# Performance work log

Hardware: AMD Instinct MI355X
Metric: run time of the kernel (lower is better)

Reference implementation:

```python
import jax, jax.numpy as jnp
import numpy as np

N, E, F_IN, F_OUT, PERIODS = 40000, 640000, 64, 128, 12


def setup_inputs() -> dict:
    key = jax.random.key(0)
    ks = jax.random.split(key, 24)
    def w(k, shape):
        return jax.random.normal(k, shape, jnp.float32) * 0.05
    inp = {
        "X": jax.random.normal(ks[0], (N, F_IN, PERIODS), jnp.float32),
        "edge_index": jax.random.randint(ks[1], (2, E), 0, N),
        "edge_weight": jax.random.uniform(ks[2], (E,), jnp.float32),
        "attention": jax.random.uniform(ks[3], (PERIODS,), jnp.float32),
    }
    for idx, g in enumerate(["i", "f", "c", "o"]):
        inp[f"W_x{g}"] = w(ks[4 + 4 * idx], (F_IN, F_OUT))
        inp[f"b_x{g}"] = jnp.zeros((F_OUT,), jnp.float32)
        inp[f"W_h{g}"] = w(ks[5 + 4 * idx], (2 * F_OUT, F_OUT))
        inp[f"b_h{g}"] = jnp.zeros((F_OUT,), jnp.float32)
    return inp


def reference(X, edge_index, edge_weight, attention,
              W_xi, b_xi, W_hi, b_hi,
              W_xf, b_xf, W_hf, b_hf,
              W_xc, b_xc, W_hc, b_hc,
              W_xo, b_xo, W_ho, b_ho):
    n = X.shape[0]
    # GCN normalization with self-loops: D^-1/2 (A + I) D^-1/2
    loops = jnp.arange(n)
    rows = jnp.concatenate([edge_index[0], loops])  # sources
    cols = jnp.concatenate([edge_index[1], loops])  # targets
    wts = jnp.concatenate([edge_weight, jnp.ones((n,), X.dtype)])
    deg = jax.ops.segment_sum(wts, cols, num_segments=n)
    dinv = jnp.where(deg > 0, jax.lax.rsqrt(deg), 0.0)
    norm = dinv[rows] * wts * dinv[cols]  # [E+N]

    def gcn(x, W, b):
        xw = x @ W  # [N, F_OUT]
        agg = jax.ops.segment_sum(norm[:, None] * xw[rows], cols, num_segments=n)
        return agg + b

    probs = jax.nn.softmax(attention)
    H0 = jnp.zeros((n, W_hi.shape[1]), X.dtype)
    C0 = jnp.zeros_like(H0)
    Xp = jnp.moveaxis(X, 2, 0)  # [periods, N, F_IN]

    def step(carry, xs):
        H, C, Hacc = carry
        x_t, p = xs
        def gate(Wx, bx, Wh, bh):
            return jnp.concatenate([gcn(x_t, Wx, bx), H], axis=1) @ Wh + bh
        I = jax.nn.sigmoid(gate(W_xi, b_xi, W_hi, b_hi))
        F = jax.nn.sigmoid(gate(W_xf, b_xf, W_hf, b_hf))
        Ct = jnp.tanh(gate(W_xc, b_xc, W_hc, b_hc))
        O = jax.nn.sigmoid(gate(W_xo, b_xo, W_ho, b_ho))
        C_new = F * C + I * Ct
        H_new = O * jnp.tanh(C_new)
        return (H_new, C_new, Hacc + p * H_new), None

    (H, C, Hacc), _ = jax.lax.scan(step, (H0, C0, H0), (Xp, probs))
    return Hacc
```

## Files before the change

### kernel.cpp

```cpp
#include <hip/hip_runtime.h>

typedef __bf16 bf16_t;
typedef bf16_t bf16x4 __attribute__((ext_vector_type(4)));
typedef bf16_t bf16x8 __attribute__((ext_vector_type(8)));
typedef float floatx4 __attribute__((ext_vector_type(4)));

#define F_INq 64
#define F_OUTq 128
#define PERIODSq 12
#define XROW (F_INq * PERIODSq)

__global__ __launch_bounds__(256) void k_init(float* deg, int* counts, int N) {
  int i = blockIdx.x * 256 + threadIdx.x;
  if (i < N) { deg[i] = 1.0f; counts[i] = 0; }
}

__global__ __launch_bounds__(256) void k_accum(const int* __restrict__ ei, const float* __restrict__ ew,
                                               float* deg, int* counts, int E) {
  int e = blockIdx.x * 256 + threadIdx.x;
  if (e < E) {
    int c = ei[E + e];
    atomicAdd(&deg[c], ew[e]);
    atomicAdd(&counts[c], 1);
  }
}

__global__ __launch_bounds__(256) void k_dinv(float* deg, int N) {
  int i = blockIdx.x * 256 + threadIdx.x;
  if (i < N) { float d = deg[i]; deg[i] = d > 0.0f ? rsqrtf(d) : 0.0f; }
}

__global__ __launch_bounds__(256) void k_scanA(const int* __restrict__ counts, float* __restrict__ deg,
                                               int* __restrict__ bsum, int N) {
  __shared__ int ws[4];
  int b = blockIdx.x, t = threadIdx.x;
  int base = b * 1024 + t * 4;
  int s = 0;
  if (base + 3 < N) {
    int4 c = *(const int4*)(counts + base);
    s = c.x + c.y + c.z + c.w;
  } else {
    for (int k = 0; k < 4; ++k) if (base + k < N) s += counts[base + k];
  }
#pragma unroll
  for (int k = 0; k < 4; ++k) {
    int idx = base + k;
    if (idx < N) { float d = deg[idx]; deg[idx] = d > 0.0f ? rsqrtf(d) : 0.0f; }
  }
  for (int off = 1; off < 64; off <<= 1) s += __shfl_xor(s, off);
  int lane = t & 63, w = t >> 6;
  if (lane == 0) ws[w] = s;
  __syncthreads();
  if (t == 0) bsum[b] = ws[0] + ws[1] + ws[2] + ws[3];
}

__global__ __launch_bounds__(256) void k_scanC(const int* __restrict__ counts, const int* __restrict__ bsum,
                                               int* __restrict__ offs, int* __restrict__ cursor, int N, int nb) {
  __shared__ int ws[4];
  int b = blockIdx.x, t = threadIdx.x;
  int base = b * 1024 + t * 4;
  int c0_ = 0, c1_ = 0, c2_ = 0, c3_ = 0;
  if (base + 3 < N) {
    int4 c = *(const int4*)(counts + base);
    c0_ = c.x; c1_ = c.y; c2_ = c.z; c3_ = c.w;
  } else {
    if (base < N) c0_ = counts[base];
    if (base + 1 < N) c1_ = counts[base + 1];
    if (base + 2 < N) c2_ = counts[base + 2];
    if (base + 3 < N) c3_ = counts[base + 3];
  }
  int tot = c0_ + c1_ + c2_ + c3_;
  int lane = t & 63, w = t >> 6;
  int inc = tot;
  for (int off = 1; off < 64; off <<= 1) {
    int u = __shfl_up(inc, off);
    if (lane >= off) inc += u;
  }
  if (lane == 63) ws[w] = inc;
  __syncthreads();
  int wb = 0;
  for (int i = 0; i < b; ++i) wb += bsum[i];
  for (int i = 0; i < w; ++i) wb += ws[i];
  int e = wb + inc - tot;
  if (base < N)     { offs[base] = e;                 cursor[base] = e; }
  if (base + 1 < N) { int o = e + c0_;                offs[base + 1] = o; cursor[base + 1] = o; }
  if (base + 2 < N) { int o = e + c0_ + c1_;          offs[base + 2] = o; cursor[base + 2] = o; }
  if (base + 3 < N) { int o = e + c0_ + c1_ + c2_;    offs[base + 3] = o; cursor[base + 3] = o; }
  if (b == nb - 1 && t == 0) {
    int tt2 = 0;
    for (int i = 0; i < nb - 1; ++i) tt2 += bsum[i];
    offs[N] = tt2 + ws[0] + ws[1] + ws[2] + ws[3];
  }
}

__global__ __launch_bounds__(1024) void k_scan(const int* __restrict__ counts, int* __restrict__ offs,
                                               int* __restrict__ cursor, int N) {
  __shared__ int sd[1024];
  int t = threadIdx.x;
  int CH = (N + 1023) >> 10;
  int base = t * CH;
  int sum = 0;
  for (int i = 0; i < CH; ++i) { int idx = base + i; if (idx < N) sum += counts[idx]; }
  sd[t] = sum;
  __syncthreads();
  for (int off = 1; off < 1024; off <<= 1) {
    int v = (t >= off) ? sd[t - off] : 0;
    __syncthreads();
    sd[t] += v;
    __syncthreads();
  }
  int run = sd[t] - sum;
  for (int i = 0; i < CH; ++i) {
    int idx = base + i;
    if (idx < N) { offs[idx] = run; cursor[idx] = run; run += counts[idx]; }
  }
  if (t == 1023) offs[N] = sd[1023];
}

__global__ __launch_bounds__(256) void k_scatter(const int* __restrict__ ei, const float* __restrict__ ew,
                                                 const float* __restrict__ dinv, int* cursor,
                                                 int* __restrict__ csr_src, float* __restrict__ csr_nrm, int E) {
  int e = blockIdx.x * 256 + threadIdx.x;
  if (e < E) {
    int r = ei[e], c = ei[E + e];
    int p = atomicAdd(&cursor[c], 1);
    csr_src[p] = r;
    csr_nrm[p] = dinv[r] * ew[e] * dinv[c];
  }
}

__global__ __launch_bounds__(256) void k_prew(
    const float* __restrict__ Wxi, const float* __restrict__ Whi,
    const float* __restrict__ Wxf, const float* __restrict__ Whf,
    const float* __restrict__ Wxc, const float* __restrict__ Whc,
    const float* __restrict__ Wxo, const float* __restrict__ Who,
    const float* __restrict__ bxi, const float* __restrict__ bhi,
    const float* __restrict__ bxf, const float* __restrict__ bhf,
    const float* __restrict__ bxc, const float* __restrict__ bhc,
    const float* __restrict__ bxo, const float* __restrict__ bho,
    const float* __restrict__ att,
    bf16_t* __restrict__ WbT, float* __restrict__ bcomb, float* __restrict__ probs) {
  const int WT = 512 * 192;
  int gid = blockIdx.x * 256 + threadIdx.x;
  if (gid < WT) {
    int col = gid / 192, k = gid % 192;
    int g = col >> 7, j = col & 127;
    const float* Wx = g == 0 ? Wxi : g == 1 ? Wxf : g == 2 ? Wxc : Wxo;
    const float* Wh = g == 0 ? Whi : g == 1 ? Whf : g == 2 ? Whc : Who;
    float s;
    if (k < 64) {
      s = 0.0f;
      for (int kk = 0; kk < 128; ++kk) s += Wx[k * 128 + kk] * Wh[kk * 128 + j];
    } else {
      s = Wh[(k + 64) * 128 + j];
    }
    WbT[(size_t)col * 192 + k] = (bf16_t)s;
  } else if (gid < WT + 512) {
    int cc = gid - WT;
    int g = cc >> 7, j = cc & 127;
    const float* bx = g == 0 ? bxi : g == 1 ? bxf : g == 2 ? bxc : bxo;
    const float* bh = g == 0 ? bhi : g == 1 ? bhf : g == 2 ? bhc : bho;
    const float* Wh = g == 0 ? Whi : g == 1 ? Whf : g == 2 ? Whc : Who;
    float s = bh[j];
    for (int kk = 0; kk < 128; ++kk) s += bx[kk] * Wh[kk * 128 + j];
    bcomb[cc] = s;
  } else if (gid == WT + 512) {
    float m = att[0];
    for (int i = 1; i < PERIODSq; ++i) m = fmaxf(m, att[i]);
    float e[PERIODSq], s = 0.0f;
    for (int i = 0; i < PERIODSq; ++i) { e[i] = __expf(att[i] - m); s += e[i]; }
    for (int i = 0; i < PERIODSq; ++i) probs[i] = e[i] / s;
  }
}

__global__ __launch_bounds__(256) void k_mid(
    const int* __restrict__ ei, const float* __restrict__ ew, const float* __restrict__ dinv,
    int* cursor, int* __restrict__ csr_src, float* __restrict__ csr_nrm, int E,
    const float* __restrict__ Wxi, const float* __restrict__ Whi,
    const float* __restrict__ Wxf, const float* __restrict__ Whf,
    const float* __restrict__ Wxc, const float* __restrict__ Whc,
    const float* __restrict__ Wxo, const float* __restrict__ Who,
    const float* __restrict__ bxi, const float* __restrict__ bhi,
    const float* __restrict__ bxf, const float* __restrict__ bhf,
    const float* __restrict__ bxc, const float* __restrict__ bhc,
    const float* __restrict__ bxo, const float* __restrict__ bho,
    const float* __restrict__ att,
    bf16_t* __restrict__ WbT, float* __restrict__ bcomb, float* __restrict__ probs,
    const float* __restrict__ X, bf16_t* __restrict__ Xb,
    int nbScatter, int nbPrew) {
  __shared__ float lds[XROW];
  const int b = blockIdx.x, tid = threadIdx.x;
  if (b < nbScatter) {
    int e = b * 256 + tid;
    if (e < E) {
      int r = ei[e], c = ei[E + e];
      int p = atomicAdd(&cursor[c], 1);
      csr_src[p] = r;
      csr_nrm[p] = dinv[r] * ew[e] * dinv[c];
    }
    return;
  }
  if (b < nbScatter + nbPrew) {
    const int WT = 512 * 192;
    int gid = (b - nbScatter) * 256 + tid;
    if (gid < WT) {
      int col = gid / 192, k = gid % 192;
      int g = col >> 7, j = col & 127;
      const float* Wx = g == 0 ? Wxi : g == 1 ? Wxf : g == 2 ? Wxc : Wxo;
      const float* Wh = g == 0 ? Whi : g == 1 ? Whf : g == 2 ? Whc : Who;
      float s;
      if (k < 64) {
        s = 0.0f;
        for (int kk = 0; kk < 128; ++kk) s += Wx[k * 128 + kk] * Wh[kk * 128 + j];
      } else {
        s = Wh[(k + 64) * 128 + j];
      }
      WbT[(size_t)col * 192 + k] = (bf16_t)s;
    } else if (gid < WT + 512) {
      int cc = gid - WT;
      int g = cc >> 7, j = cc & 127;
      const float* bx = g == 0 ? bxi : g == 1 ? bxf : g == 2 ? bxc : bxo;
      const float* bh = g == 0 ? bhi : g == 1 ? bhf : g == 2 ? bhc : bho;
      const float* Wh = g == 0 ? Whi : g == 1 ? Whf : g == 2 ? Whc : Who;
      float s = bh[j];
      for (int kk = 0; kk < 128; ++kk) s += bx[kk] * Wh[kk * 128 + j];
      bcomb[cc] = s;
    } else if (gid == WT + 512) {
      float m = att[0];
      for (int i = 1; i < PERIODSq; ++i) m = fmaxf(m, att[i]);
      float e[PERIODSq], s = 0.0f;
      for (int i = 0; i < PERIODSq; ++i) { e[i] = __expf(att[i] - m); s += e[i]; }
      for (int i = 0; i < PERIODSq; ++i) probs[i] = e[i] / s;
    }
    return;
  }
  const int n = b - nbScatter - nbPrew;
  if (tid < 192) {
    const float4* Xr = (const float4*)(X + (size_t)n * XROW);
    float4 v = Xr[tid];
    lds[tid * 4 + 0] = v.x;
    lds[tid * 4 + 1] = v.y;
    lds[tid * 4 + 2] = v.z;
    lds[tid * 4 + 3] = v.w;
  }
  __syncthreads();
  if (tid < 192) {
    const int o = tid * 4;
    bf16x4 r;
#pragma unroll
    for (int k = 0; k < 4; ++k) {
      int oo = o + k;
      int tt = oo >> 6, f = oo & 63;
      r[k] = (bf16_t)lds[f * PERIODSq + tt];
    }
    *(bf16x4*)(Xb + (size_t)n * XROW + o) = r;
  }
}

__global__ __launch_bounds__(192) void k_xpose(const float* __restrict__ X, bf16_t* __restrict__ Xb) {
  __shared__ float lds[XROW];
  const int n = blockIdx.x, tid = threadIdx.x;
  const float4* Xr = (const float4*)(X + (size_t)n * XROW);
  float4 v = Xr[tid];
  lds[tid * 4 + 0] = v.x;
  lds[tid * 4 + 1] = v.y;
  lds[tid * 4 + 2] = v.z;
  lds[tid * 4 + 3] = v.w;
  __syncthreads();
  const int o = tid * 4;
  bf16x4 r;
#pragma unroll
  for (int k = 0; k < 4; ++k) {
    int oo = o + k;
    int tt = oo >> 6, f = oo & 63;
    r[k] = (bf16_t)lds[f * PERIODSq + tt];
  }
  *(bf16x4*)(Xb + (size_t)n * XROW + o) = r;
}

__global__ __launch_bounds__(256) void k_agg2(const bf16_t* __restrict__ Xb, const int* __restrict__ csr_src,
                                              const float* __restrict__ csr_nrm, const int* __restrict__ offs,
                                              const float* __restrict__ dinv, bf16_t* __restrict__ Xagg, int N) {
  const int node = blockIdx.x * 4 + (threadIdx.x >> 6);
  const int lane = threadIdx.x & 63;
  const int s0 = offs[node], s1 = offs[node + 1];
  floatx4 a0 = {0.f, 0.f, 0.f, 0.f}, a1 = a0, a2 = a0;
  int e = s0;
  for (; e + 8 <= s1; e += 8) {
    bf16x4 v[8][3];
    float nn[8];
#pragma unroll
    for (int u = 0; u < 8; ++u) {
      int s = csr_src[e + u];
      nn[u] = csr_nrm[e + u];
      const bf16x4* xp = (const bf16x4*)(Xb + (size_t)s * XROW) + lane;
      v[u][0] = xp[0]; v[u][1] = xp[64]; v[u][2] = xp[128];
    }
#pragma unroll
    for (int u = 0; u < 8; ++u) {
#pragma unroll
      for (int k = 0; k < 4; ++k) {
        a0[k] += nn[u] * (float)v[u][0][k];
        a1[k] += nn[u] * (float)v[u][1][k];
        a2[k] += nn[u] * (float)v[u][2][k];
      }
    }
  }
  for (; e < s1; ++e) {
    int s = csr_src[e];
    float nr = csr_nrm[e];
    const bf16x4* xp = (const bf16x4*)(Xb + (size_t)s * XROW) + lane;
    bf16x4 v0 = xp[0], v1 = xp[64], v2 = xp[128];
#pragma unroll
    for (int k = 0; k < 4; ++k) {
      a0[k] += nr * (float)v0[k];
      a1[k] += nr * (float)v1[k];
      a2[k] += nr * (float)v2[k];
    }
  }
  float dc = dinv[node];
  float self = dc * dc;
  const bf16x4* xc = (const bf16x4*)(Xb + (size_t)node * XROW) + lane;
  {
    bf16x4 v0 = xc[0], v1 = xc[64], v2 = xc[128];
#pragma unroll
    for (int k = 0; k < 4; ++k) {
      a0[k] += self * (float)v0[k];
      a1[k] += self * (float)v1[k];
      a2[k] += self * (float)v2[k];
    }
  }
  const int f4 = lane & 15, tq = lane >> 4;
  floatx4 accs[3] = {a0, a1, a2};
#pragma unroll
  for (int j = 0; j < 3; ++j) {
    int tt = tq + 4 * j;
    bf16x4 r;
#pragma unroll
    for (int k = 0; k < 4; ++k) r[k] = (bf16_t)accs[j][k];
    *(bf16x4*)(Xagg + ((size_t)tt * N + node) * 64 + f4 * 4) = r;
  }
}

__global__ __launch_bounds__(256) void k_agg(const float* __restrict__ X, const int* __restrict__ csr_src,
                                             const float* __restrict__ csr_nrm, const int* __restrict__ offs,
                                             const float* __restrict__ dinv, bf16_t* __restrict__ Xagg, int N) {
  int c = blockIdx.x;
  int tid = threadIdx.x;
  int s0 = offs[c], s1 = offs[c + 1];
  const int i0 = tid, i1 = tid + 256, i2 = tid + 512;
  float a0 = 0.f, a1 = 0.f, a2 = 0.f;
  for (int e = s0; e < s1; ++e) {
    int s = csr_src[e];
    float nr = csr_nrm[e];
    const float* xp = X + (size_t)s * XROW;
    a0 += nr * xp[i0]; a1 += nr * xp[i1]; a2 += nr * xp[i2];
  }
  float dc = dinv[c];
  float self = dc * dc;
  const float* xc = X + (size_t)c * XROW;
  a0 += self * xc[i0]; a1 += self * xc[i1]; a2 += self * xc[i2];
  __shared__ float lds[XROW];
  lds[i0] = a0; lds[i1] = a1; lds[i2] = a2;
  __syncthreads();
  for (int o = tid; o < XROW; o += 256) {
    int tt = o >> 6, f = o & 63;
    Xagg[(size_t)tt * N * 64 + (size_t)c * 64 + f] = (bf16_t)lds[f * PERIODSq + tt];
  }
}

__global__ __launch_bounds__(512, 2) void k_gate_all(const bf16_t* __restrict__ Xagg,
                                                     const bf16_t* __restrict__ WbT,
                                                     const float* __restrict__ bcomb,
                                                     const float* __restrict__ probs,
                                                     float* __restrict__ out, int N) {
  __shared__ __align__(16) char Hs[2][32 * 256];
  const int tid = threadIdx.x;
  const int lane = tid & 63, w = tid >> 6;
  const int q = lane >> 4, c0 = lane & 15;
  const int n0 = blockIdx.x * 32;
  const int swz = c0 & 7;

  bf16x8 Wf[4][6];
#pragma unroll
  for (int g = 0; g < 4; ++g) {
    const bf16_t* wp = WbT + (size_t)((g * 8 + w) * 16 + c0) * 192;
#pragma unroll
    for (int ks = 0; ks < 6; ++ks) Wf[g][ks] = *(const bf16x8*)(wp + ks * 32 + q * 8);
  }
  floatx4 bv[4];
#pragma unroll
  for (int g = 0; g < 4; ++g) bv[g] = *(const floatx4*)(bcomb + g * 128 + w * 16 + q * 4);
  float pr[PERIODSq];
#pragma unroll
  for (int i = 0; i < PERIODSq; ++i) pr[i] = probs[i];

  floatx4 Cst[2], Ha[2];
#pragma unroll
  for (int rt = 0; rt < 2; ++rt) {
    Cst[rt] = (floatx4){0.f, 0.f, 0.f, 0.f};
    Ha[rt] = (floatx4){0.f, 0.f, 0.f, 0.f};
  }

  const bf16_t* Xrow0 = Xagg + (size_t)(n0 + c0) * 64 + q * 8;
  const bf16_t* Xrow1 = Xagg + (size_t)(n0 + 16 + c0) * 64 + q * 8;

  bf16x8 Xf0 = *(const bf16x8*)(Xrow0);
  bf16x8 Xf1 = *(const bf16x8*)(Xrow0 + 32);
  bf16x8 Xf2 = *(const bf16x8*)(Xrow1);
  bf16x8 Xf3 = *(const bf16x8*)(Xrow1 + 32);

  floatx4 accA[2][4], accB[2][4];
#pragma unroll
  for (int g = 0; g < 4; ++g) {
    accA[0][g] = __builtin_amdgcn_mfma_f32_16x16x32_bf16(Wf[g][0], Xf0, bv[g], 0, 0, 0);
    accA[0][g] = __builtin_amdgcn_mfma_f32_16x16x32_bf16(Wf[g][1], Xf1, accA[0][g], 0, 0, 0);
    accA[1][g] = __builtin_amdgcn_mfma_f32_16x16x32_bf16(Wf[g][0], Xf2, bv[g], 0, 0, 0);
    accA[1][g] = __builtin_amdgcn_mfma_f32_16x16x32_bf16(Wf[g][1], Xf3, accA[1][g], 0, 0, 0);
  }

  const float NL2E = -1.44269504f;
  const float T2L2E = 2.88539008f;

#define PERIOD(T, AC, AN, RB, WB, DO_H, DO_NEXT)                                                      \
  do {                                                                                                \
    if (DO_NEXT) {                                                                                    \
      const size_t toff_ = (size_t)((T) + 1) * N * 64;                                                \
      Xf0 = *(const bf16x8*)(Xrow0 + toff_);                                                          \
      Xf1 = *(const bf16x8*)(Xrow0 + toff_ + 32);                                                     \
      Xf2 = *(const bf16x8*)(Xrow1 + toff_);                                                          \
      Xf3 = *(const bf16x8*)(Xrow1 + toff_ + 32);                                                     \
    }                                                                                                 \
    if (DO_H) {                                                                                       \
      _Pragma("unroll") for (int ks = 0; ks < 4; ++ks) {                                              \
        bf16x8 B0 = *(const bf16x8*)(&Hs[RB][(c0) * 256 + (((4 * ks + q) ^ swz) << 4)]);              \
        bf16x8 B1 = *(const bf16x8*)(&Hs[RB][(16 + c0) * 256 + (((4 * ks + q) ^ swz) << 4)]);         \
        _Pragma("unroll") for (int g = 0; g < 4; ++g) {                                               \
          AC[0][g] = __builtin_amdgcn_mfma_f32_16x16x32_bf16(Wf[g][ks + 2], B0, AC[0][g], 0, 0, 0);   \
          AC[1][g] = __builtin_amdgcn_mfma_f32_16x16x32_bf16(Wf[g][ks + 2], B1, AC[1][g], 0, 0, 0);   \
        }                                                                                             \
      }                                                                                               \
    }                                                                                                 \
    const float pt_ = pr[T];                                                                          \
    _Pragma("unroll") for (int rt = 0; rt < 2; ++rt) {                                                \
      bf16x4 hv_;                                                                                     \
      _Pragma("unroll") for (int r = 0; r < 4; ++r) {                                                 \
        float pI = AC[rt][0][r], pF = AC[rt][1][r], pC = AC[rt][2][r], pO = AC[rt][3][r];             \
        float I_ = __builtin_amdgcn_rcpf(1.0f + __builtin_amdgcn_exp2f(pI * NL2E));                   \
        float F_ = __builtin_amdgcn_rcpf(1.0f + __builtin_amdgcn_exp2f(pF * NL2E));                   \
        float Ct_ = fmaf(-2.0f, __builtin_amdgcn_rcpf(1.0f + __builtin_amdgcn_exp2f(pC * T2L2E)), 1.0f); \
        float O_ = __builtin_amdgcn_rcpf(1.0f + __builtin_amdgcn_exp2f(pO * NL2E));                   \
        float Cn_ = fmaf(F_, Cst[rt][r], I_ * Ct_);                                                   \
        Cst[rt][r] = Cn_;                                                                             \
        float tC_ = fmaf(-2.0f, __builtin_amdgcn_rcpf(1.0f + __builtin_amdgcn_exp2f(Cn_ * T2L2E)), 1.0f); \
        float Hn_ = O_ * tC_;                                                                         \
        Ha[rt][r] = fmaf(pt_, Hn_, Ha[rt][r]);                                                        \
        hv_[r] = (bf16_t)Hn_;                                                                         \
      }                                                                                               \
      *(bf16x4*)(&Hs[WB][(rt * 16 + c0) * 256 + (((2 * w + (q >> 1)) ^ swz) << 4) + ((q & 1) * 8)]) = hv_; \
    }                                                                                                 \
    if (DO_NEXT) {                                                                                    \
      _Pragma("unroll") for (int g = 0; g < 4; ++g) {                                                 \
        AN[0][g] = __builtin_amdgcn_mfma_f32_16x16x32_bf16(Wf[g][0], Xf0, bv[g], 0, 0, 0);            \
        AN[0][g] = __builtin_amdgcn_mfma_f32_16x16x32_bf16(Wf[g][1], Xf1, AN[0][g], 0, 0, 0);         \
        AN[1][g] = __builtin_amdgcn_mfma_f32_16x16x32_bf16(Wf[g][0], Xf2, bv[g], 0, 0, 0);            \
        AN[1][g] = __builtin_amdgcn_mfma_f32_16x16x32_bf16(Wf[g][1], Xf3, AN[1][g], 0, 0, 0);         \
      }                                                                                               \
    }                                                                                                 \
    __syncthreads();                                                                                  \
  } while (0)

  PERIOD(0, accA, accB, 1, 0, 0, 1);
  for (int tt = 1; tt <= 9; tt += 2) {
    PERIOD(tt, accB, accA, 0, 1, 1, 1);
    PERIOD(tt + 1, accA, accB, 1, 0, 1, 1);
  }
  PERIOD(11, accB, accA, 0, 1, 1, 0);
#undef PERIOD

#pragma unroll
  for (int rt = 0; rt < 2; ++rt) {
    int row = n0 + rt * 16 + c0;
    *(floatx4*)(out + (size_t)row * 128 + w * 16 + q * 4) = Ha[rt];
  }
}

extern "C" void kernel_launch(void* const* d_in, const int* in_sizes, int n_in,
                              void* d_out, int out_size, void* d_ws, size_t ws_size,
                              hipStream_t stream) {
  const float* X = (const float*)d_in[0];
  const int* ei = (const int*)d_in[1];
  const float* ew = (const float*)d_in[2];
  const float* att = (const float*)d_in[3];
  const float* Wxi = (const float*)d_in[4];
  const float* bxi = (const float*)d_in[5];
  const float* Whi = (const float*)d_in[6];
  const float* bhi = (const float*)d_in[7];
  const float* Wxf = (const float*)d_in[8];
  const float* bxf = (const float*)d_in[9];
  const float* Whf = (const float*)d_in[10];
  const float* bhf = (const float*)d_in[11];
  const float* Wxc = (const float*)d_in[12];
  const float* bxc = (const float*)d_in[13];
  const float* Whc = (const float*)d_in[14];
  const float* bhc = (const float*)d_in[15];
  const float* Wxo = (const float*)d_in[16];
  const float* bxo = (const float*)d_in[17];
  const float* Who = (const float*)d_in[18];
  const float* bho = (const float*)d_in[19];
  float* out = (float*)d_out;

  const int N = in_sizes[0] / XROW;
  const int E = in_sizes[2];

  char* base = (char*)d_ws;
  size_t off = 0;
  auto carve = [&](size_t bytes) {
    char* r = base + off;
    off += (bytes + 255) & ~(size_t)255;
    return (void*)r;
  };
  float* deg = (float*)carve((size_t)N * 4);
  int* counts = (int*)carve((size_t)N * 4);
  int* offs = (int*)carve((size_t)(N + 1) * 4);
  int* cursor = (int*)carve((size_t)(N + 1) * 4);
  int* csr_src = (int*)carve((size_t)E * 4);
  float* csr_nrm = (float*)carve((size_t)E * 4);
  bf16_t* WbT = (bf16_t*)carve((size_t)512 * 192 * 2);
  float* bcomb = (float*)carve(512 * 4);
  float* probs = (float*)carve(64);
  int* bsum = (int*)carve(64 * 4);
  bf16_t* Xagg = (bf16_t*)carve((size_t)PERIODSq * N * 64 * 2);
  bf16_t* Xb = (bf16_t*)carve((size_t)N * XROW * 2);
  const bool use_bf16 = (off <= ws_size) && ((N & 3) == 0);

  k_init<<<(N + 255) / 256, 256, 0, stream>>>(deg, counts, N);
  k_accum<<<(E + 255) / 256, 256, 0, stream>>>(ei, ew, deg, counts, E);
  const int nb = (N + 1023) >> 10;
  if (nb <= 64) {
    k_scanA<<<nb, 256, 0, stream>>>(counts, deg, bsum, N);
    k_scanC<<<nb, 256, 0, stream>>>(counts, bsum, offs, cursor, N, nb);
  } else {
    k_dinv<<<(N + 255) / 256, 256, 0, stream>>>(deg, N);
    k_scan<<<1, 1024, 0, stream>>>(counts, offs, cursor, N);
  }

  const int nbScatter = (E + 255) / 256;
  const int nbPrew = (512 * 192 + 512 + 1 + 255) / 256;
  if (use_bf16) {
    k_mid<<<nbScatter + nbPrew + N, 256, 0, stream>>>(
        ei, ew, deg, cursor, csr_src, csr_nrm, E,
        Wxi, Whi, Wxf, Whf, Wxc, Whc, Wxo, Who,
        bxi, bhi, bxf, bhf, bxc, bhc, bxo, bho, att, WbT, bcomb, probs,
        X, Xb, nbScatter, nbPrew);
    k_agg2<<<N / 4, 256, 0, stream>>>(Xb, csr_src, csr_nrm, offs, deg, Xagg, N);
  } else {
    k_scatter<<<nbScatter, 256, 0, stream>>>(ei, ew, deg, cursor, csr_src, csr_nrm, E);
    k_prew<<<nbPrew, 256, 0, stream>>>(
        Wxi, Whi, Wxf, Whf, Wxc, Whc, Wxo, Who,
        bxi, bhi, bxf, bhf, bxc, bhc, bxo, bho, att, WbT, bcomb, probs);
    k_agg<<<N, 256, 0, stream>>>(X, csr_src, csr_nrm, offs, deg, Xagg, N);
  }

  k_gate_all<<<N / 32, 512, 0, stream>>>(Xagg, WbT, bcomb, probs, out, N);
}
```

Before: 612.0 us.

## Fuse graph aggregation into gated LSTM kernel, overlapping gathers with MFMA

Replaces the separate aggregation kernel, which wrote a per-period aggregated X buffer to global memory, with a fused kernel. Each block of 32 nodes gathers neighbour features for 4 periods at a time into LDS while running the gate MFMAs and LSTM update for the current period. This removes the global round-trip of the aggregated tensor and one kernel launch, and hides gather latency behind compute. In exchange, register pressure and per-block work grow, and the fallback path now aliases Xagg to Xb. It also requires N to be a multiple of 32.

New measurement: 1.096 ms. 1.79x slower.

```diff
diff --git a/kernel.cpp b/kernel.cpp
--- a/kernel.cpp
+++ b/kernel.cpp
@@ -257,91 +257,6 @@
   }
 }
 
-__global__ __launch_bounds__(192) void k_xpose(const float* __restrict__ X, bf16_t* __restrict__ Xb) {
-  __shared__ float lds[XROW];
-  const int n = blockIdx.x, tid = threadIdx.x;
-  const float4* Xr = (const float4*)(X + (size_t)n * XROW);
-  float4 v = Xr[tid];
-  lds[tid * 4 + 0] = v.x;
-  lds[tid * 4 + 1] = v.y;
-  lds[tid * 4 + 2] = v.z;
-  lds[tid * 4 + 3] = v.w;
-  __syncthreads();
-  const int o = tid * 4;
-  bf16x4 r;
-#pragma unroll
-  for (int k = 0; k < 4; ++k) {
-    int oo = o + k;
-    int tt = oo >> 6, f = oo & 63;
-    r[k] = (bf16_t)lds[f * PERIODSq + tt];
-  }
-  *(bf16x4*)(Xb + (size_t)n * XROW + o) = r;
-}
-
-__global__ __launch_bounds__(256) void k_agg2(const bf16_t* __restrict__ Xb, const int* __restrict__ csr_src,
-                                              const float* __restrict__ csr_nrm, const int* __restrict__ offs,
-                                              const float* __restrict__ dinv, bf16_t* __restrict__ Xagg, int N) {
-  const int node = blockIdx.x * 4 + (threadIdx.x >> 6);
-  const int lane = threadIdx.x & 63;
-  const int s0 = offs[node], s1 = offs[node + 1];
-  floatx4 a0 = {0.f, 0.f, 0.f, 0.f}, a1 = a0, a2 = a0;
-  int e = s0;
-  for (; e + 8 <= s1; e += 8) {
-    bf16x4 v[8][3];
-    float nn[8];
-#pragma unroll
-    for (int u = 0; u < 8; ++u) {
-      int s = csr_src[e + u];
-      nn[u] = csr_nrm[e + u];
-      const bf16x4* xp = (const bf16x4*)(Xb + (size_t)s * XROW) + lane;
-      v[u][0] = xp[0]; v[u][1] = xp[64]; v[u][2] = xp[128];
-    }
-#pragma unroll
-    for (int u = 0; u < 8; ++u) {
-#pragma unroll
-      for (int k = 0; k < 4; ++k) {
-        a0[k] += nn[u] * (float)v[u][0][k];
-        a1[k] += nn[u] * (float)v[u][1][k];
-        a2[k] += nn[u] * (float)v[u][2][k];
-      }
-    }
-  }
-  for (; e < s1; ++e) {
-    int s = csr_src[e];
-    float nr = csr_nrm[e];
-    const bf16x4* xp = (const bf16x4*)(Xb + (size_t)s * XROW) + lane;
-    bf16x4 v0 = xp[0], v1 = xp[64], v2 = xp[128];
-#pragma unroll
-    for (int k = 0; k < 4; ++k) {
-      a0[k] += nr * (float)v0[k];
-      a1[k] += nr * (float)v1[k];
-      a2[k] += nr * (float)v2[k];
-    }
-  }
-  float dc = dinv[node];
-  float self = dc * dc;
-  const bf16x4* xc = (const bf16x4*)(Xb + (size_t)node * XROW) + lane;
-  {
-    bf16x4 v0 = xc[0], v1 = xc[64], v2 = xc[128];
-#pragma unroll
-    for (int k = 0; k < 4; ++k) {
-      a0[k] += self * (float)v0[k];
-      a1[k] += self * (float)v1[k];
-      a2[k] += self * (float)v2[k];
-    }
-  }
-  const int f4 = lane & 15, tq = lane >> 4;
-  floatx4 accs[3] = {a0, a1, a2};
-#pragma unroll
-  for (int j = 0; j < 3; ++j) {
-    int tt = tq + 4 * j;
-    bf16x4 r;
-#pragma unroll
-    for (int k = 0; k < 4; ++k) r[k] = (bf16_t)accs[j][k];
-    *(bf16x4*)(Xagg + ((size_t)tt * N + node) * 64 + f4 * 4) = r;
-  }
-}
-
 __global__ __launch_bounds__(256) void k_agg(const float* __restrict__ X, const int* __restrict__ csr_src,
                                              const float* __restrict__ csr_nrm, const int* __restrict__ offs,
                                              const float* __restrict__ dinv, bf16_t* __restrict__ Xagg, int N) {
@@ -477,6 +392,191 @@
   }
   PERIOD(11, accB, accA, 0, 1, 1, 0);
 #undef PERIOD
+
+#pragma unroll
+  for (int rt = 0; rt < 2; ++rt) {
+    int row = n0 + rt * 16 + c0;
+    *(floatx4*)(out + (size_t)row * 128 + w * 16 + q * 4) = Ha[rt];
+  }
+}
+
+__global__ __launch_bounds__(512, 2) void k_gate_fused(
+    const bf16_t* __restrict__ Xb, const int* __restrict__ csr_src, const float* __restrict__ csr_nrm,
+    const int* __restrict__ offs, const float* __restrict__ dinv,
+    const bf16_t* __restrict__ WbT, const float* __restrict__ bcomb, const float* __restrict__ probs,
+    float* __restrict__ out, int N) {
+  __shared__ __align__(16) char Hs[2][32 * 256];
+  __shared__ __align__(16) char Xl[2][32 * 512];
+  __shared__ float probsS[16];
+  const int tid = threadIdx.x;
+  const int lane = tid & 63, w = tid >> 6;
+  const int q = lane >> 4, c0 = lane & 15;
+  const int n0 = blockIdx.x * 32;
+  const int swz = c0 & 7;
+  const int xkey = swz << 2;
+
+  if (tid < PERIODSq) probsS[tid] = probs[tid];
+
+  bf16x8 Wf[4][6];
+#pragma unroll
+  for (int g = 0; g < 4; ++g) {
+    const bf16_t* wp = WbT + (size_t)((g * 8 + w) * 16 + c0) * 192;
+#pragma unroll
+    for (int ks = 0; ks < 6; ++ks) Wf[g][ks] = *(const bf16x8*)(wp + ks * 32 + q * 8);
+  }
+  floatx4 bv[4];
+#pragma unroll
+  for (int g = 0; g < 4; ++g) bv[g] = *(const floatx4*)(bcomb + g * 128 + w * 16 + q * 4);
+
+  const int gbase = n0 + 4 * w;
+  const int eStart = offs[gbase];
+  const int b1 = offs[gbase + 1], b2 = offs[gbase + 2], b3 = offs[gbase + 3];
+  const int eTot = offs[gbase + 4];
+  float sf[4];
+#pragma unroll
+  for (int i = 0; i < 4; ++i) { float dv = dinv[gbase + i]; sf[i] = dv * dv; }
+
+  floatx4 accN[4];
+  bf16x4 xv[8];
+  float nr[8];
+  int nu[8];
+  bf16x4 sxv[4];
+  int e = eStart;
+#pragma unroll
+  for (int i = 0; i < 4; ++i) accN[i] = (floatx4){0.f, 0.f, 0.f, 0.f};
+
+#define G_ISSUE(SOFF)                                                                  \
+  _Pragma("unroll") for (int u = 0; u < 8; ++u) {                                      \
+    int idx_ = e + u;                                                                  \
+    if (idx_ < eTot) {                                                                 \
+      int s_ = csr_src[idx_];                                                          \
+      nr[u] = csr_nrm[idx_];                                                           \
+      nu[u] = (idx_ >= b1) + (idx_ >= b2) + (idx_ >= b3);                              \
+      xv[u] = *(const bf16x4*)(Xb + (size_t)s_ * XROW + (SOFF) + lane * 4);            \
+    } else {                                                                           \
+      nr[u] = 0.0f; nu[u] = 0;                                                         \
+      xv[u] = (bf16x4){(bf16_t)0.0f, (bf16_t)0.0f, (bf16_t)0.0f, (bf16_t)0.0f};       \
+    }                                                                                  \
+  }
+
+#define G_DRAIN()                                                                      \
+  _Pragma("unroll") for (int u = 0; u < 8; ++u) {                                      \
+    float nv_ = nr[u]; bf16x4 xx_ = xv[u]; int t_ = nu[u];                             \
+    if (t_ == 0) { _Pragma("unroll") for (int k = 0; k < 4; ++k) accN[0][k] += nv_ * (float)xx_[k]; } \
+    else if (t_ == 1) { _Pragma("unroll") for (int k = 0; k < 4; ++k) accN[1][k] += nv_ * (float)xx_[k]; } \
+    else if (t_ == 2) { _Pragma("unroll") for (int k = 0; k < 4; ++k) accN[2][k] += nv_ * (float)xx_[k]; } \
+    else { _Pragma("unroll") for (int k = 0; k < 4; ++k) accN[3][k] += nv_ * (float)xx_[k]; } \
+  }                                                                                    \
+  e += 8;
+
+#define G_SELF(SOFF)                                                                   \
+  _Pragma("unroll") for (int i = 0; i < 4; ++i)                                        \
+    sxv[i] = *(const bf16x4*)(Xb + (size_t)(gbase + i) * XROW + (SOFF) + lane * 4);
+
+#define G_WRITE(BUF)                                                                   \
+  _Pragma("unroll") for (int i = 0; i < 4; ++i) {                                      \
+    int row_ = 4 * w + i;                                                              \
+    bf16x4 hx_;                                                                        \
+    _Pragma("unroll") for (int k = 0; k < 4; ++k)                                      \
+      hx_[k] = (bf16_t)(accN[i][k] + sf[i] * (float)sxv[i][k]);                        \
+    *(bf16x4*)(&Xl[BUF][row_ * 512 + ((((lane >> 1) ^ ((row_ & 7) << 2)) << 4) + (lane & 1) * 8)]) = hx_; \
+    accN[i] = (floatx4){0.f, 0.f, 0.f, 0.f};                                           \
+  }                                                                                    \
+  e = eStart;
+
+  while (e < eTot) { G_ISSUE(0); G_DRAIN(); }
+  G_SELF(0);
+  G_WRITE(0);
+
+  floatx4 Cst[2], Ha[2];
+#pragma unroll
+  for (int rt = 0; rt < 2; ++rt) {
+    Cst[rt] = (floatx4){0.f, 0.f, 0.f, 0.f};
+    Ha[rt] = (floatx4){0.f, 0.f, 0.f, 0.f};
+  }
+  __syncthreads();
+
+  const float NL2E = -1.44269504f;
+  const float T2L2E = 2.88539008f;
+
+#define GPER(T, GAT, LAST)                                                                            \
+  do {                                                                                                \
+    const int XBuf = ((T) >> 2) & 1;                                                                  \
+    const int tl = (T) & 3;                                                                           \
+    const int soff_ = (((T) >> 2) + 1) * 256;                                                         \
+    if (GAT) { G_ISSUE(soff_); }                                                                      \
+    floatx4 acc[2][4];                                                                                \
+    {                                                                                                 \
+      bf16x8 X00 = *(const bf16x8*)(&Xl[XBuf][c0 * 512 + (((tl * 8 + q) ^ xkey) << 4)]);              \
+      bf16x8 X01 = *(const bf16x8*)(&Xl[XBuf][c0 * 512 + (((tl * 8 + 4 + q) ^ xkey) << 4)]);          \
+      bf16x8 X10 = *(const bf16x8*)(&Xl[XBuf][(16 + c0) * 512 + (((tl * 8 + q) ^ xkey) << 4)]);       \
+      bf16x8 X11 = *(const bf16x8*)(&Xl[XBuf][(16 + c0) * 512 + (((tl * 8 + 4 + q) ^ xkey) << 4)]);   \
+      _Pragma("unroll") for (int g = 0; g < 4; ++g) {                                                 \
+        acc[0][g] = __builtin_amdgcn_mfma_f32_16x16x32_bf16(Wf[g][0], X00, bv[g], 0, 0, 0);           \
+        acc[0][g] = __builtin_amdgcn_mfma_f32_16x16x32_bf16(Wf[g][1], X01, acc[0][g], 0, 0, 0);       \
+        acc[1][g] = __builtin_amdgcn_mfma_f32_16x16x32_bf16(Wf[g][0], X10, bv[g], 0, 0, 0);           \
+        acc[1][g] = __builtin_amdgcn_mfma_f32_16x16x32_bf16(Wf[g][1], X11, acc[1][g], 0, 0, 0);       \
+      }                                                                                               \
+    }                                                                                                 \
+    if (GAT) { G_DRAIN(); G_ISSUE(soff_); }                                                           \
+    if ((T) > 0) {                                                                                    \
+      const int RB = ((T) & 1) ^ 1;                                                                   \
+      _Pragma("unroll") for (int ks = 0; ks < 4; ++ks) {                                              \
+        bf16x8 B0 = *(const bf16x8*)(&Hs[RB][c0 * 256 + (((4 * ks + q) ^ swz) << 4)]);                \
+        bf16x8 B1 = *(const bf16x8*)(&Hs[RB][(16 + c0) * 256 + (((4 * ks + q) ^ swz) << 4)]);         \
+        _Pragma("unroll") for (int g = 0; g < 4; ++g) {                                               \
+          acc[0][g] = __builtin_amdgcn_mfma_f32_16x16x32_bf16(Wf[g][ks + 2], B0, acc[0][g], 0, 0, 0); \
+          acc[1][g] = __builtin_amdgcn_mfma_f32_16x16x32_bf16(Wf[g][ks + 2], B1, acc[1][g], 0, 0, 0); \
+        }                                                                                             \
+      }                                                                                               \
+    }                                                                                                 \
+    {                                                                                                 \
+      const int WB = (T) & 1;                                                                         \
+      const float pt_ = probsS[T];                                                                    \
+      _Pragma("unroll") for (int rt = 0; rt < 2; ++rt) {                                              \
+        bf16x4 hv_;                                                                                   \
+        _Pragma("unroll") for (int r = 0; r < 4; ++r) {                                               \
+          float pI = acc[rt][0][r], pF = acc[rt][1][r], pC = acc[rt][2][r], pO = acc[rt][3][r];       \
+          float I_ = __builtin_amdgcn_rcpf(1.0f + __builtin_amdgcn_exp2f(pI * NL2E));                 \
+          float F_ = __builtin_amdgcn_rcpf(1.0f + __builtin_amdgcn_exp2f(pF * NL2E));                 \
+          float Ct_ = fmaf(-2.0f, __builtin_amdgcn_rcpf(1.0f + __builtin_amdgcn_exp2f(pC * T2L2E)), 1.0f); \
+          float O_ = __builtin_amdgcn_rcpf(1.0f + __builtin_amdgcn_exp2f(pO * NL2E));                 \
+          float Cn_ = fmaf(F_, Cst[rt][r], I_ * Ct_);                                                 \
+          Cst[rt][r] = Cn_;                                                                           \
+          float tC_ = fmaf(-2.0f, __builtin_amdgcn_rcpf(1.0f + __builtin_amdgcn_exp2f(Cn_ * T2L2E)), 1.0f); \
+          float Hn_ = O_ * tC_;                                                                       \
+          Ha[rt][r] = fmaf(pt_, Hn_, Ha[rt][r]);                                                      \
+          hv_[r] = (bf16_t)Hn_;                                                                       \
+        }                                                                                             \
+        *(bf16x4*)(&Hs[WB][(rt * 16 + c0) * 256 + (((2 * w + (q >> 1)) ^ swz) << 4) + ((q & 1) * 8)]) = hv_; \
+      }                                                                                               \
+    }                                                                                                 \
+    if (GAT) { G_DRAIN(); }                                                                           \
+    if (LAST) {                                                                                       \
+      G_SELF(soff_);                                                                                  \
+      while (e < eTot) { G_ISSUE(soff_); G_DRAIN(); }                                                 \
+      G_WRITE((((T) >> 2) + 1) & 1);                                                                  \
+    }                                                                                                 \
+    __syncthreads();                                                                                  \
+  } while (0)
+
+  GPER(0, 1, 0);
+  GPER(1, 1, 0);
+  GPER(2, 1, 0);
+  GPER(3, 1, 1);
+  GPER(4, 1, 0);
+  GPER(5, 1, 0);
+  GPER(6, 1, 0);
+  GPER(7, 1, 1);
+  GPER(8, 0, 0);
+  GPER(9, 0, 0);
+  GPER(10, 0, 0);
+  GPER(11, 0, 0);
+#undef GPER
+#undef G_ISSUE
+#undef G_DRAIN
+#undef G_SELF
+#undef G_WRITE
 
 #pragma unroll
   for (int rt = 0; rt < 2; ++rt) {
@@ -530,9 +630,9 @@
   float* bcomb = (float*)carve(512 * 4);
   float* probs = (float*)carve(64);
   int* bsum = (int*)carve(64 * 4);
-  bf16_t* Xagg = (bf16_t*)carve((size_t)PERIODSq * N * 64 * 2);
   bf16_t* Xb = (bf16_t*)carve((size_t)N * XROW * 2);
-  const bool use_bf16 = (off <= ws_size) && ((N & 3) == 0);
+  bf16_t* Xagg = Xb;
+  const bool use_bf16 = (off <= ws_size) && ((N & 31) == 0);
 
   k_init<<<(N + 255) / 256, 256, 0, stream>>>(deg, counts, N);
   k_accum<<<(E + 255) / 256, 256, 0, stream>>>(ei, ew, deg, counts, E);
@@ -553,14 +653,13 @@
         Wxi, Whi, Wxf, Whf, Wxc, Whc, Wxo, Who,
         bxi, bhi, bxf, bhf, bxc, bhc, bxo, bho, att, WbT, bcomb, probs,
         X, Xb, nbScatter, nbPrew);
-    k_agg2<<<N / 4, 256, 0, stream>>>(Xb, csr_src, csr_nrm, offs, deg, Xagg, N);
+    k_gate_fused<<<N / 32, 512, 0, stream>>>(Xb, csr_src, csr_nrm, offs, deg, WbT, bcomb, probs, out, N);
   } else {
     k_scatter<<<nbScatter, 256, 0, stream>>>(ei, ew, deg, cursor, csr_src, csr_nrm, E);
     k_prew<<<nbPrew, 256, 0, stream>>>(
         Wxi, Whi, Wxf, Whf, Wxc, Whc, Wxo, Who,
         bxi, bhi, bxf, bhf, bxc, bhc, bxo, bho, att, WbT, bcomb, probs);
     k_agg<<<N, 256, 0, stream>>>(X, csr_src, csr_nrm, offs, deg, Xagg, N);
-  }
-
-  k_gate_all<<<N / 32, 512, 0, stream>>>(Xagg, WbT, bcomb, probs, out, N);
-}
+    k_gate_all<<<N / 32, 512, 0, stream>>>(Xagg, WbT, bcomb, probs, out, N);
+  }
+}
```
